# Optimization experiments

Hardware: AMD Instinct MI355X
Metric: run time of the kernel (lower is better)

Reference implementation:

```python
import jax, jax.numpy as jnp
import numpy as np

B, C, H, W = 4, 64, 64, 64
C8 = C // 8


def cl_attention(x, gamma):
    # DANet CAM-style channel attention: [B,C,H,W] -> [B,C,H,W]
    b, c, h, w = x.shape
    xf = x.reshape(b, c, h * w)                       # b c n
    energy = jnp.einsum('bcn,bdn->bcd', xf, xf)       # b c c
    energy = jnp.max(energy, axis=-1, keepdims=True) - energy
    attn = jax.nn.softmax(energy, axis=-1)
    out = jnp.einsum('bcd,bdn->bcn', attn, xf).reshape(b, c, h, w)
    return gamma * out + x


def setup_inputs() -> dict:
    key = jax.random.key(0)
    ks = jax.random.split(key, 8)
    s = 0.02
    return {
        'cnn_feat': jax.random.normal(ks[0], (B, C, H, W), jnp.float32),
        'vit_feat': jax.random.normal(ks[1], (B, C, H, W), jnp.float32),
        'Wq': jax.random.normal(ks[2], (C8, C), jnp.float32) * s,   # 1x1 conv kernel
        'bq': jnp.zeros((C8,), jnp.float32),
        'Wk': jax.random.normal(ks[3], (C8, C), jnp.float32) * s,
        'bk': jnp.zeros((C8,), jnp.float32),
        'Wv': jax.random.normal(ks[4], (C, C), jnp.float32) * s,
        'bv': jnp.zeros((C,), jnp.float32),
        'gamma': jnp.zeros((1,), jnp.float32),
        'gamma_cla_cnn': jnp.zeros((1,), jnp.float32),
        'gamma_cla_vit': jnp.zeros((1,), jnp.float32),
    }


def reference(cnn_feat, vit_feat, Wq, bq, Wk, bk, Wv, bv, gamma,
              gamma_cla_cnn, gamma_cla_vit):
    b, c, h, w = cnn_feat.shape
    n = h * w

    cnn_att = cl_attention(cnn_feat, gamma_cla_cnn)   # b c h w
    vit_att = cl_attention(vit_feat, gamma_cla_vit)   # b c h w

    # query: 1x1 conv -> view(b, C8, n) -> permute -> (b, n, C8)
    q = jnp.einsum('bchw,oc->bhwo', cnn_att, Wq).reshape(b, n, -1) + bq

    # vit: rearrange 'b c h w -> b (h w) c'
    vit_flat = vit_att.reshape(b, c, n).transpose(0, 2, 1)          # b n c
    k = vit_flat @ Wk.T + bk                                        # b n C8
    v = vit_flat @ Wv.T + bv                                        # b n C

    energy = jnp.einsum('bqd,bkd->bqk', q, k)                       # b n n
    attn = jax.nn.softmax(energy, axis=-1)
    out = jnp.einsum('bqk,bkc->bqc', attn, v)                       # b n c
    out = out.transpose(0, 2, 1).reshape(b, c, h, w)                # 'b (h w) c -> b c h w'
    return gamma * out + cnn_feat
```

## Files before the change

### kernel.cpp

```cpp
#include <hip/hip_runtime.h>
#include <hip/hip_bf16.h>

#define BSZ 4
#define CC 64
#define NN 4096
#define CN (CC*NN)
#define BCN (BSZ*CN)

typedef __attribute__((ext_vector_type(4))) float    f4v;
typedef __attribute__((ext_vector_type(4))) int      i4v;
typedef __attribute__((ext_vector_type(2))) int      i2v;
typedef __attribute__((ext_vector_type(2))) unsigned u2v;
typedef __attribute__((ext_vector_type(8))) short    s8v;

#define DPP_F(x_, ctrl_) __builtin_bit_cast(float, \
    __builtin_amdgcn_update_dpp(0, __builtin_bit_cast(int, (float)(x_)), (ctrl_), 0xf, 0xf, true))
#define QP_X1 0xB1

__device__ __forceinline__ unsigned pack_bf16(float lo, float hi) {
    unsigned l = __builtin_bit_cast(unsigned, lo);
    unsigned h = __builtin_bit_cast(unsigned, hi);
    return (h & 0xFFFF0000u) | (l >> 16);
}
__device__ __forceinline__ unsigned pack2(float lo, float hi) {
    float2 f2; f2.x = lo; f2.y = hi;
    __hip_bfloat162 h = __float22bfloat162_rn(f2);
    unsigned u;
    __builtin_memcpy(&u, &h, 4);
    return u;
}
__device__ __forceinline__ float blo(int d) {
    return __builtin_bit_cast(float, (unsigned)d << 16);
}
__device__ __forceinline__ float bhi(int d) {
    return __builtin_bit_cast(float, (unsigned)d & 0xFFFF0000u);
}

__global__ __launch_bounds__(256) void gram_k(const float* __restrict__ cnn,
                                              const float* __restrict__ vit,
                                              float* __restrict__ part) {
    __shared__ __align__(16) float sXT[64*68];
    int t = threadIdx.x;
    int blk = blockIdx.x;
    int ch = blk & 63, b = (blk >> 6) & 3, i2 = blk >> 8;
    const float* X = (i2 ? vit : cnn) + b * CN;
    int n0 = ch * 64;
#pragma unroll
    for (int j = 0; j < 4; j++) {
        int idx = t + j * 256;
        int c = idx >> 4, n4 = idx & 15;
        f4v val = *(const f4v*)&X[c * NN + n0 + n4 * 4];
        int base = (n4 * 4) * 68 + c;
        sXT[base]       = val[0];
        sXT[base + 68]  = val[1];
        sXT[base + 136] = val[2];
        sXT[base + 204] = val[3];
    }
    __syncthreads();
    int tc = (t & 15) * 4, td = (t >> 4) * 4;
    f4v acc[4];
#pragma unroll
    for (int i = 0; i < 4; i++) acc[i] = (f4v){0.f, 0.f, 0.f, 0.f};
    for (int k = 0; k < 64; k++) {
        f4v a  = *(const f4v*)&sXT[k * 68 + tc];
        f4v bb = *(const f4v*)&sXT[k * 68 + td];
#pragma unroll
        for (int i = 0; i < 4; i++) acc[i] += a[i] * bb;
    }
    float* dst = part + ch * 32768 + (i2 * 4 + b) * 4096;
#pragma unroll
    for (int i = 0; i < 4; i++) *(f4v*)&dst[(tc + i) * 64 + td] = acc[i];
}

__global__ void gred_k(const float* __restrict__ part, float* __restrict__ G) {
    int row = blockIdx.x;
    int d = threadIdx.x;
    float s = 0.f;
#pragma unroll 8
    for (int ch = 0; ch < 64; ch++) s += part[ch * 32768 + row * 64 + d];
    float mn = s;
#pragma unroll
    for (int off = 1; off < 64; off <<= 1) mn = fminf(mn, __shfl_xor(mn, off));
    float e = __expf(mn - s);
    float sm = e;
#pragma unroll
    for (int off = 1; off < 64; off <<= 1) sm += __shfl_xor(sm, off);
    G[row * 64 + d] = e / sm;
}

__global__ __launch_bounds__(256) void weff_k(const float* __restrict__ G,
                                              const float* __restrict__ Wq,
                                              const float* __restrict__ Wk,
                                              const float* __restrict__ Wv,
                                              const float* __restrict__ gcnn,
                                              const float* __restrict__ gvit,
                                              ushort* __restrict__ WeffB) {
    __shared__ float sA[8192];
    __shared__ float sWt[1024];
    int t = threadIdx.x;
    int b = blockIdx.x / 5, tile = blockIdx.x % 5;
    for (int i = t; i < 4096; i += 256) {
        sA[i]        = G[b * 4096 + i];
        sA[4096 + i] = G[(4 + b) * 4096 + i];
    }
    __syncthreads();
    float gc = *gcnn, gv = *gvit;
#pragma unroll
    for (int k = 0; k < 4; k++) {
        int idx = k * 256 + t;
        int r = idx >> 6, c = idx & 63;
        const float* Wrow; const float* A; float g;
        if (tile == 0) {
            if (r < 8) { Wrow = Wq + r * 64;       A = sA;        g = gc; }
            else       { Wrow = Wk + (r - 8) * 64; A = sA + 4096; g = gv; }
        } else         { Wrow = Wv + ((tile - 1) * 16 + r) * 64; A = sA + 4096; g = gv; }
        float s = 0.f;
#pragma unroll 8
        for (int d = 0; d < 64; d++) s += Wrow[d] * A[d * 64 + c];
        sWt[idx] = g * s + Wrow[c];
    }
    __syncthreads();
    if (t < 128) {
        int frag = t >> 6, lane = t & 63, m = lane & 15, q4 = lane >> 4;
        i4v o;
#pragma unroll
        for (int p = 0; p < 4; p++) {
            int c0 = frag * 32 + q4 * 8 + 2 * p;
            o[p] = (int)pack_bf16(sWt[m * 64 + c0], sWt[m * 64 + c0 + 1]);
        }
        *(i4v*)&WeffB[(size_t)(b * 10 + tile * 2 + frag) * 512 + lane * 8] = o;
    }
}

__global__ __launch_bounds__(256) void qkv_k(const float* __restrict__ cnn,
                                             const float* __restrict__ vit,
                                             const ushort* __restrict__ WeffB,
                                             const float* __restrict__ bq,
                                             const float* __restrict__ bk,
                                             const float* __restrict__ bv,
                                             ushort* __restrict__ qb, ushort* __restrict__ kb,
                                             ushort* __restrict__ vT) {
    int t = threadIdx.x;
    int b = blockIdx.x >> 6, n0 = (blockIdx.x & 63) * 64;
    int w = t >> 6, lane = t & 63, c15 = lane & 15, q4 = lane >> 4;
    int n = n0 + w * 16 + c15;
    const float LOG2E = 1.44269504f;

    s8v A[10];
    const ushort* WB = WeffB + (size_t)b * 5120 + lane * 8;
#pragma unroll
    for (int i = 0; i < 10; i++)
        A[i] = __builtin_bit_cast(s8v, *(const i4v*)(WB + (size_t)i * 512));

    s8v Bc[2], Bv[2];
#pragma unroll
    for (int f = 0; f < 2; f++) {
        i4v pc, pv;
#pragma unroll
        for (int p = 0; p < 4; p++) {
            int c0 = f * 32 + q4 * 8 + p * 2;
            size_t a0 = (size_t)b * CN + (size_t)c0 * NN + n;
            pc[p] = (int)pack_bf16(cnn[a0], cnn[a0 + NN]);
            pv[p] = (int)pack_bf16(vit[a0], vit[a0 + NN]);
        }
        Bc[f] = __builtin_bit_cast(s8v, pc);
        Bv[f] = __builtin_bit_cast(s8v, pv);
    }

    f4v acc = *(const f4v*)(bq + (q4 & 1) * 4);
    acc = __builtin_amdgcn_mfma_f32_16x16x32_bf16(A[0], Bc[0], acc, 0, 0, 0);
    acc = __builtin_amdgcn_mfma_f32_16x16x32_bf16(A[1], Bc[1], acc, 0, 0, 0);
    if (q4 < 2) {
        unsigned d0 = pack_bf16(acc[0] * LOG2E, acc[1] * LOG2E);
        unsigned d1 = pack_bf16(acc[2] * LOG2E, acc[3] * LOG2E);
        unsigned long long v = ((unsigned long long)d1 << 32) | d0;
        *(unsigned long long*)&qb[(size_t)(b * NN + n) * 8 + q4 * 4] = v;
    }
    acc = *(const f4v*)(bk + (q4 & 1) * 4);
    acc = __builtin_amdgcn_mfma_f32_16x16x32_bf16(A[0], Bv[0], acc, 0, 0, 0);
    acc = __builtin_amdgcn_mfma_f32_16x16x32_bf16(A[1], Bv[1], acc, 0, 0, 0);
    if (q4 >= 2) {
        unsigned d0 = pack_bf16(acc[0], acc[1]), d1 = pack_bf16(acc[2], acc[3]);
        unsigned long long v = ((unsigned long long)d1 << 32) | d0;
        *(unsigned long long*)&kb[(size_t)(b * NN + n) * 8 + (q4 - 2) * 4] = v;
    }
#pragma unroll
    for (int tile = 1; tile < 5; tile++) {
        acc = *(const f4v*)(bv + (tile - 1) * 16 + q4 * 4);
        acc = __builtin_amdgcn_mfma_f32_16x16x32_bf16(A[tile * 2],     Bv[0], acc, 0, 0, 0);
        acc = __builtin_amdgcn_mfma_f32_16x16x32_bf16(A[tile * 2 + 1], Bv[1], acc, 0, 0, 0);
#pragma unroll
        for (int r = 0; r < 4; r++) {
            float other = DPP_F(acc[r], QP_X1);
            unsigned pkd = (lane & 1) ? pack_bf16(other, acc[r])
                                      : pack_bf16(acc[r], other);
            if (!(lane & 1)) {
                int row = (tile - 1) * 16 + q4 * 4 + r;
                *(unsigned*)&vT[(size_t)(b * 64 + row) * NN + n] = pkd;
            }
        }
    }
}

__global__ __launch_bounds__(256, 2) void flash_k(const ushort* __restrict__ qb,
                                                  const ushort* __restrict__ kb,
                                                  const ushort* __restrict__ vT,
                                                  ushort* __restrict__ pOT,
                                                  float* __restrict__ pl) {
    __shared__ __align__(16) ushort Vlds[2 * 64 * 72];
    int t = threadIdx.x;
    int lane = t & 63, w = t >> 6;
    int c15 = lane & 15, q4 = lane >> 4;
    int blk = blockIdx.x;
    int s = blk >> 6, b = (blk >> 4) & 3, q0 = (blk & 15) * 256;

    s8v qB[4];
#pragma unroll
    for (int g = 0; g < 4; g++) {
        i4v qa = (i4v){0, 0, 0, 0};
        if (q4 == 0)
            qa = *(const i4v*)(qb + (size_t)(b * NN + q0 + w * 64 + g * 16 + c15) * 8);
        qB[g] = __builtin_bit_cast(s8v, qa);
    }

    f4v accO[4][4];
#pragma unroll
    for (int g = 0; g < 4; g++)
#pragma unroll
        for (int nt = 0; nt < 4; nt++) accO[g][nt] = (f4v){0.f, 0.f, 0.f, 0.f};
    float lacc[4] = {0.f, 0.f, 0.f, 0.f};

    const ushort* kbb = kb + (size_t)b * NN * 8 + (size_t)c15 * 8;

    int r = t >> 2, chk = t & 3;
    const ushort* vsrc = vT + (size_t)(b * 64 + r) * NN + chk * 16;
    int vdstoff = r * 72 + 32 * (chk >> 1) + 4 * (chk & 1);
    int vreadoff = c15 * 72 + 8 * q4;

    int kbase = s * 512;
    i4v bk_cur[4];
#pragma unroll
    for (int nt = 0; nt < 4; nt++)
        bk_cur[nt] = *(const i4v*)(kbb + (size_t)(kbase + nt * 16) * 8);
    i4v v0 = *(const i4v*)(vsrc + kbase);
    i4v v1 = *(const i4v*)(vsrc + kbase + 8);

    for (int kt = 0; kt < 8; kt++) {
        int k0 = kbase + kt * 64;
        ushort* vd = Vlds + (kt & 1) * 4608 + vdstoff;
        *(i2v*)(vd + 0)  = (i2v){v0[0], v0[1]};
        *(i2v*)(vd + 8)  = (i2v){v0[2], v0[3]};
        *(i2v*)(vd + 16) = (i2v){v1[0], v1[1]};
        *(i2v*)(vd + 24) = (i2v){v1[2], v1[3]};
        __syncthreads();

        const ushort* vb = Vlds + (kt & 1) * 4608 + vreadoff;
        i4v vA[2][4];
#pragma unroll
        for (int F = 0; F < 2; F++)
#pragma unroll
            for (int nt = 0; nt < 4; nt++)
                vA[F][nt] = *(const i4v*)(vb + nt * 16 * 72 + 32 * F);

        i4v bk_nxt[4];
        if (kt < 7) {
            v0 = *(const i4v*)(vsrc + k0 + 64);
            v1 = *(const i4v*)(vsrc + k0 + 64 + 8);
#pragma unroll
            for (int nt = 0; nt < 4; nt++)
                bk_nxt[nt] = *(const i4v*)(kbb + (size_t)(k0 + 64 + nt * 16) * 8);
        }

#pragma unroll
        for (int gp = 0; gp < 2; gp++) {
            f4v z = (f4v){0.f, 0.f, 0.f, 0.f};
            f4v S[2][4];
#pragma unroll
            for (int gg = 0; gg < 2; gg++)
#pragma unroll
                for (int nt = 0; nt < 4; nt++)
                    S[gg][nt] = __builtin_amdgcn_mfma_f32_16x16x32_bf16(
                        __builtin_bit_cast(s8v, bk_cur[nt]), qB[gp * 2 + gg],
                        z, 0, 0, 0);

            s8v Bp[2][2];
#pragma unroll
            for (int gg = 0; gg < 2; gg++) {
                f4v p[4];
                float ps = 0.f;
#pragma unroll
                for (int nt = 0; nt < 4; nt++)
#pragma unroll
                    for (int rr = 0; rr < 4; rr++) {
                        p[nt][rr] = __builtin_amdgcn_exp2f(S[gg][nt][rr]);
                        ps += p[nt][rr];
                    }
#pragma unroll
                for (int F = 0; F < 2; F++) {
                    i4v bp;
                    bp[0] = (int)pack2(p[2 * F][0],     p[2 * F][1]);
                    bp[1] = (int)pack2(p[2 * F][2],     p[2 * F][3]);
                    bp[2] = (int)pack2(p[2 * F + 1][0], p[2 * F + 1][1]);
                    bp[3] = (int)pack2(p[2 * F + 1][2], p[2 * F + 1][3]);
                    Bp[gg][F] = __builtin_bit_cast(s8v, bp);
                }
                lacc[gp * 2 + gg] += ps;
            }

#pragma unroll
            for (int F = 0; F < 2; F++)
#pragma unroll
                for (int gg = 0; gg < 2; gg++)
#pragma unroll
                    for (int nt = 0; nt < 4; nt++)
                        accO[gp * 2 + gg][nt] =
                            __builtin_amdgcn_mfma_f32_16x16x32_bf16(
                                __builtin_bit_cast(s8v, vA[F][nt]), Bp[gg][F],
                                accO[gp * 2 + gg][nt], 0, 0, 0);
        }
        if (kt < 7) {
#pragma unroll
            for (int nt = 0; nt < 4; nt++) bk_cur[nt] = bk_nxt[nt];
        }
    }

#pragma unroll
    for (int g = 0; g < 4; g++) {
        lacc[g] += __shfl_xor(lacc[g], 16);
        lacc[g] += __shfl_xor(lacc[g], 32);
    }

#pragma unroll
    for (int g = 0; g < 4; g++) {
        int qg = q0 + w * 64 + g * 16 + c15;
#pragma unroll
        for (int nt = 0; nt < 4; nt++) {
            int cg = nt * 4 + q4;
            u2v d;
            d[0] = pack2(accO[g][nt][0], accO[g][nt][1]);
            d[1] = pack2(accO[g][nt][2], accO[g][nt][3]);
            *(u2v*)&pOT[((size_t)((s * 4 + b) * 16 + cg) * NN + qg) * 4] = d;
        }
        if (q4 == 0)
            pl[(size_t)(s * 4 + b) * NN + qg] = lacc[g];
    }
}

__global__ __launch_bounds__(256) void comb_k(const ushort* __restrict__ pOT,
                                              const float* __restrict__ pl,
                                              const float* __restrict__ cnn,
                                              const float* __restrict__ gamma,
                                              float* __restrict__ out) {
    int t = threadIdx.x;
    int b = blockIdx.x >> 6, n0 = (blockIdx.x & 63) * 64;
    int nq = t & 15, cl = t >> 4;
    int n = n0 + nq * 4;
    f4v L = (f4v){0.f, 0.f, 0.f, 0.f};
#pragma unroll
    for (int s = 0; s < 8; s++)
        L += *(const f4v*)&pl[(size_t)(s * 4 + b) * NN + n];
    float g = *gamma;
    f4v rv;
#pragma unroll
    for (int j = 0; j < 4; j++) rv[j] = g / L[j];

    f4v Oc[4];
#pragma unroll
    for (int cc = 0; cc < 4; cc++) Oc[cc] = (f4v){0.f, 0.f, 0.f, 0.f};
#pragma unroll
    for (int s = 0; s < 8; s++) {
        const ushort* src = pOT + ((size_t)((s * 4 + b) * 16 + cl) * NN + n) * 4;
        i4v a  = *(const i4v*)src;
        i4v bb = *(const i4v*)(src + 8);
        Oc[0][0] += blo(a[0]);  Oc[1][0] += bhi(a[0]);
        Oc[2][0] += blo(a[1]);  Oc[3][0] += bhi(a[1]);
        Oc[0][1] += blo(a[2]);  Oc[1][1] += bhi(a[2]);
        Oc[2][1] += blo(a[3]);  Oc[3][1] += bhi(a[3]);
        Oc[0][2] += blo(bb[0]); Oc[1][2] += bhi(bb[0]);
        Oc[2][2] += blo(bb[1]); Oc[3][2] += bhi(bb[1]);
        Oc[0][3] += blo(bb[2]); Oc[1][3] += bhi(bb[2]);
        Oc[2][3] += blo(bb[3]); Oc[3][3] += bhi(bb[3]);
    }
#pragma unroll
    for (int cc = 0; cc < 4; cc++) {
        size_t gi = (size_t)(b * 64 + cl * 4 + cc) * NN + n;
        f4v cv = *(const f4v*)&cnn[gi];
        *(f4v*)&out[gi] = Oc[cc] * rv + cv;
    }
}

extern "C" void kernel_launch(void* const* d_in, const int* in_sizes, int n_in,
                              void* d_out, int out_size, void* d_ws, size_t ws_size,
                              hipStream_t stream) {
    const float* cnn  = (const float*)d_in[0];
    const float* vit  = (const float*)d_in[1];
    const float* Wq   = (const float*)d_in[2];
    const float* bq   = (const float*)d_in[3];
    const float* Wk   = (const float*)d_in[4];
    const float* bk   = (const float*)d_in[5];
    const float* Wv   = (const float*)d_in[6];
    const float* bv   = (const float*)d_in[7];
    const float* gam  = (const float*)d_in[8];
    const float* gcnn = (const float*)d_in[9];
    const float* gvit = (const float*)d_in[10];
    float* out = (float*)d_out;

    float* ws = (float*)d_ws;
    ushort* pOT   = (ushort*)ws;
    float*  part  = ws;
    float*  G     = ws + 8388608;
    ushort* WeffB = (ushort*)(ws + 8421376);
    ushort* qb    = (ushort*)(ws + 8431616);
    ushort* kb    = (ushort*)(ws + 8497152);
    ushort* vT    = (ushort*)(ws + 8562688);
    float*  pl    = ws + 9086976;

    gram_k <<<512, 256, 0, stream>>>(cnn, vit, part);
    gred_k <<<512, 64,  0, stream>>>(part, G);
    weff_k <<<20,  256, 0, stream>>>(G, Wq, Wk, Wv, gcnn, gvit, WeffB);
    qkv_k  <<<256, 256, 0, stream>>>(cnn, vit, WeffB, bq, bk, bv, qb, kb, vT);
    flash_k<<<512, 256, 0, stream>>>(qb, kb, vT, pOT, pl);
    comb_k <<<256, 256, 0, stream>>>(pOT, pl, cnn, gam, out);
}
```

Before: 129.4 us.

## Fuse split-KV combine into flash kernel via last-block counter; halve gram chunks

Measured after the change: 185.1 us. +43.1%, slower.

```diff
diff --git a/kernel.cpp b/kernel.cpp
--- a/kernel.cpp
+++ b/kernel.cpp
@@ -38,17 +38,19 @@
 
 __global__ __launch_bounds__(256) void gram_k(const float* __restrict__ cnn,
                                               const float* __restrict__ vit,
-                                              float* __restrict__ part) {
-    __shared__ __align__(16) float sXT[64*68];
+                                              float* __restrict__ part,
+                                              unsigned* __restrict__ cnt) {
+    __shared__ __align__(16) float sXT[128*68];
     int t = threadIdx.x;
     int blk = blockIdx.x;
-    int ch = blk & 63, b = (blk >> 6) & 3, i2 = blk >> 8;
+    if (blk < 64 && t == 0) cnt[blk] = 0;
+    int ch = blk & 31, b = (blk >> 5) & 3, i2 = blk >> 7;
     const float* X = (i2 ? vit : cnn) + b * CN;
-    int n0 = ch * 64;
-#pragma unroll
-    for (int j = 0; j < 4; j++) {
+    int n0 = ch * 128;
+#pragma unroll
+    for (int j = 0; j < 8; j++) {
         int idx = t + j * 256;
-        int c = idx >> 4, n4 = idx & 15;
+        int c = idx >> 5, n4 = idx & 31;
         f4v val = *(const f4v*)&X[c * NN + n0 + n4 * 4];
         int base = (n4 * 4) * 68 + c;
         sXT[base]       = val[0];
@@ -61,7 +63,7 @@
     f4v acc[4];
 #pragma unroll
     for (int i = 0; i < 4; i++) acc[i] = (f4v){0.f, 0.f, 0.f, 0.f};
-    for (int k = 0; k < 64; k++) {
+    for (int k = 0; k < 128; k++) {
         f4v a  = *(const f4v*)&sXT[k * 68 + tc];
         f4v bb = *(const f4v*)&sXT[k * 68 + td];
 #pragma unroll
@@ -77,7 +79,7 @@
     int d = threadIdx.x;
     float s = 0.f;
 #pragma unroll 8
-    for (int ch = 0; ch < 64; ch++) s += part[ch * 32768 + row * 64 + d];
+    for (int ch = 0; ch < 32; ch++) s += part[ch * 32768 + row * 64 + d];
     float mn = s;
 #pragma unroll
     for (int off = 1; off < 64; off <<= 1) mn = fminf(mn, __shfl_xor(mn, off));
@@ -206,13 +208,18 @@
                                                   const ushort* __restrict__ kb,
                                                   const ushort* __restrict__ vT,
                                                   ushort* __restrict__ pOT,
-                                                  float* __restrict__ pl) {
+                                                  float* __restrict__ pl,
+                                                  unsigned* __restrict__ cnt,
+                                                  const float* __restrict__ cnn,
+                                                  const float* __restrict__ gamma,
+                                                  float* __restrict__ out) {
     __shared__ __align__(16) ushort Vlds[2 * 64 * 72];
+    __shared__ int lastflag;
     int t = threadIdx.x;
     int lane = t & 63, w = t >> 6;
     int c15 = lane & 15, q4 = lane >> 4;
     int blk = blockIdx.x;
-    int s = blk >> 6, b = (blk >> 4) & 3, q0 = (blk & 15) * 256;
+    int s = blk >> 6, b = (blk >> 4) & 3, qc = blk & 15, q0 = qc * 256;
 
     s8v qB[4];
 #pragma unroll
@@ -344,48 +351,49 @@
         if (q4 == 0)
             pl[(size_t)(s * 4 + b) * NN + qg] = lacc[g];
     }
-}
-
-__global__ __launch_bounds__(256) void comb_k(const ushort* __restrict__ pOT,
-                                              const float* __restrict__ pl,
-                                              const float* __restrict__ cnn,
-                                              const float* __restrict__ gamma,
-                                              float* __restrict__ out) {
-    int t = threadIdx.x;
-    int b = blockIdx.x >> 6, n0 = (blockIdx.x & 63) * 64;
+
+    __threadfence();
+    if (t == 0) lastflag = (int)atomicAdd(&cnt[b * 16 + qc], 1u);
+    __syncthreads();
+    if (lastflag != 7) return;
+    __threadfence();
+
+    float gsc = *gamma;
     int nq = t & 15, cl = t >> 4;
-    int n = n0 + nq * 4;
-    f4v L = (f4v){0.f, 0.f, 0.f, 0.f};
-#pragma unroll
-    for (int s = 0; s < 8; s++)
-        L += *(const f4v*)&pl[(size_t)(s * 4 + b) * NN + n];
-    float g = *gamma;
-    f4v rv;
-#pragma unroll
-    for (int j = 0; j < 4; j++) rv[j] = g / L[j];
-
-    f4v Oc[4];
-#pragma unroll
-    for (int cc = 0; cc < 4; cc++) Oc[cc] = (f4v){0.f, 0.f, 0.f, 0.f};
-#pragma unroll
-    for (int s = 0; s < 8; s++) {
-        const ushort* src = pOT + ((size_t)((s * 4 + b) * 16 + cl) * NN + n) * 4;
-        i4v a  = *(const i4v*)src;
-        i4v bb = *(const i4v*)(src + 8);
-        Oc[0][0] += blo(a[0]);  Oc[1][0] += bhi(a[0]);
-        Oc[2][0] += blo(a[1]);  Oc[3][0] += bhi(a[1]);
-        Oc[0][1] += blo(a[2]);  Oc[1][1] += bhi(a[2]);
-        Oc[2][1] += blo(a[3]);  Oc[3][1] += bhi(a[3]);
-        Oc[0][2] += blo(bb[0]); Oc[1][2] += bhi(bb[0]);
-        Oc[2][2] += blo(bb[1]); Oc[3][2] += bhi(bb[1]);
-        Oc[0][3] += blo(bb[2]); Oc[1][3] += bhi(bb[2]);
-        Oc[2][3] += blo(bb[3]); Oc[3][3] += bhi(bb[3]);
-    }
-#pragma unroll
-    for (int cc = 0; cc < 4; cc++) {
-        size_t gi = (size_t)(b * 64 + cl * 4 + cc) * NN + n;
-        f4v cv = *(const f4v*)&cnn[gi];
-        *(f4v*)&out[gi] = Oc[cc] * rv + cv;
+#pragma unroll
+    for (int chunk = 0; chunk < 4; chunk++) {
+        int n = q0 + chunk * 64 + nq * 4;
+        f4v L = (f4v){0.f, 0.f, 0.f, 0.f};
+#pragma unroll
+        for (int ss = 0; ss < 8; ss++)
+            L += *(const f4v*)&pl[(size_t)(ss * 4 + b) * NN + n];
+        f4v rv;
+#pragma unroll
+        for (int j = 0; j < 4; j++) rv[j] = gsc / L[j];
+
+        f4v Oc[4];
+#pragma unroll
+        for (int cc = 0; cc < 4; cc++) Oc[cc] = (f4v){0.f, 0.f, 0.f, 0.f};
+#pragma unroll
+        for (int ss = 0; ss < 8; ss++) {
+            const ushort* src = pOT + ((size_t)((ss * 4 + b) * 16 + cl) * NN + n) * 4;
+            i4v a  = *(const i4v*)src;
+            i4v bb = *(const i4v*)(src + 8);
+            Oc[0][0] += blo(a[0]);  Oc[1][0] += bhi(a[0]);
+            Oc[2][0] += blo(a[1]);  Oc[3][0] += bhi(a[1]);
+            Oc[0][1] += blo(a[2]);  Oc[1][1] += bhi(a[2]);
+            Oc[2][1] += blo(a[3]);  Oc[3][1] += bhi(a[3]);
+            Oc[0][2] += blo(bb[0]); Oc[1][2] += bhi(bb[0]);
+            Oc[2][2] += blo(bb[1]); Oc[3][2] += bhi(bb[1]);
+            Oc[0][3] += blo(bb[2]); Oc[1][3] += bhi(bb[2]);
+            Oc[2][3] += blo(bb[3]); Oc[3][3] += bhi(bb[3]);
+        }
+#pragma unroll
+        for (int cc = 0; cc < 4; cc++) {
+            size_t gi = (size_t)(b * 64 + cl * 4 + cc) * NN + n;
+            f4v cv = *(const f4v*)&cnn[gi];
+            *(f4v*)&out[gi] = Oc[cc] * rv + cv;
+        }
     }
 }
 
@@ -406,19 +414,19 @@
     float* out = (float*)d_out;
 
     float* ws = (float*)d_ws;
-    ushort* pOT   = (ushort*)ws;
-    float*  part  = ws;
-    float*  G     = ws + 8388608;
-    ushort* WeffB = (ushort*)(ws + 8421376);
-    ushort* qb    = (ushort*)(ws + 8431616);
-    ushort* kb    = (ushort*)(ws + 8497152);
-    ushort* vT    = (ushort*)(ws + 8562688);
-    float*  pl    = ws + 9086976;
-
-    gram_k <<<512, 256, 0, stream>>>(cnn, vit, part);
+    ushort*   pOT   = (ushort*)ws;
+    float*    part  = ws;
+    float*    G     = ws + 8388608;
+    ushort*   WeffB = (ushort*)(ws + 8421376);
+    ushort*   qb    = (ushort*)(ws + 8431616);
+    ushort*   kb    = (ushort*)(ws + 8497152);
+    ushort*   vT    = (ushort*)(ws + 8562688);
+    float*    pl    = ws + 9086976;
+    unsigned* cnt   = (unsigned*)(ws + 9218048);
+
+    gram_k <<<256, 256, 0, stream>>>(cnn, vit, part, cnt);
     gred_k <<<512, 64,  0, stream>>>(part, G);
     weff_k <<<20,  256, 0, stream>>>(G, Wq, Wk, Wv, gcnn, gvit, WeffB);
     qkv_k  <<<256, 256, 0, stream>>>(cnn, vit, WeffB, bq, bk, bv, qb, kb, vT);
-    flash_k<<<512, 256, 0, stream>>>(qb, kb, vT, pOT, pl);
-    comb_k <<<256, 256, 0, stream>>>(pOT, pl, cnn, gam, out);
-}
+    flash_k<<<512, 256, 0, stream>>>(qb, kb, vT, pOT, pl, cnt, cnn, gam, out);
+}
```
